# Kernel tuning notes

Hardware: AMD Instinct MI355X
Metric: run time of the kernel (lower is better)

Reference implementation:

```python
import jax, jax.numpy as jnp
import numpy as np

B, F, N, J, L_LAYERS = 16, 16, 1024, 8, 3


def setup_inputs() -> dict:
    key = jax.random.key(0)
    k1, k2, k3 = jax.random.split(key, 3)
    x = jax.random.normal(k1, (B, F, N), dtype=jnp.float32)
    psi = jax.random.normal(k2, (J, N, N), dtype=jnp.float32) / np.sqrt(N)
    lowpass = jax.random.uniform(k3, (N,), dtype=jnp.float32) / N
    return {"x": x, "psi": psi, "lowpass": lowpass, "L": L_LAYERS}


def reference(x, psi, lowpass, L):
    # x: [B, F, N] graph signals; psi: [J, N, N] wavelet filterbank; lowpass: [N]
    Bs, Fs, Ns = x.shape
    # layer-0 lowpass projection: phi = x @ lowpass -> [B, F, 1]
    phi = jnp.einsum('bfn,n->bf', x, lowpass)[:, :, None]
    S_x = x[:, None, :, :]  # [B, K=1, F, N]
    for _ in range(1, L):
        # apply all J wavelets to all K branches, then abs nonlinearity
        # (branch order k-major, j-minor matches the torch cat loop)
        S_x = jnp.abs(jnp.einsum('bkfn,jnm->bkjfm', S_x, psi))
        K = S_x.shape[1] * S_x.shape[2]
        S_x = S_x.reshape(Bs, K, Fs, Ns)
        # lowpass-pool every branch: [B, F, K]
        phi_l = jnp.einsum('bkfn,n->bfk', S_x, lowpass)
        phi = jnp.concatenate([phi, phi_l], axis=2)
    return phi  # [B, F, 1 + J + J^2 + ... + J^(L-1)]
```

## Files before the change

### kernel.cpp

```cpp
#include <hip/hip_runtime.h>

#define ND 1024
#define NNE (ND*ND)

typedef float f32x4 __attribute__((ext_vector_type(4)));
typedef int i32x4 __attribute__((ext_vector_type(4)));
typedef int i32x8 __attribute__((ext_vector_type(8)));

__device__ __forceinline__ void gload_lds16(const void* g, void* l) {
  __builtin_amdgcn_global_load_lds(
      (const __attribute__((address_space(1))) void*)g,
      (__attribute__((address_space(3))) void*)l, 16, 0, 0);
}

__global__ __launch_bounds__(256)
void prep_kernel(const float* __restrict__ psi, unsigned char* __restrict__ out8,
                 const float* __restrict__ x, const float* __restrict__ lp,
                 unsigned char* __restrict__ x8, float* __restrict__ phi) {
  __shared__ __align__(16) unsigned char T[128 * 144];
  __shared__ float ws[4];
  const int blk = blockIdx.x;
  const int tid = threadIdx.x;

  if (blk >= 512) {
    int row = blk - 512;
    if (tid >= 1 && tid < 73) phi[row * 73 + tid] = 0.f;
    float4 v = reinterpret_cast<const float4*>(x + (size_t)row * ND)[tid];
    float4 l = reinterpret_cast<const float4*>(lp)[tid];
    int pk = __builtin_amdgcn_cvt_pk_fp8_f32(v.x, v.y, 0, false);
    pk = __builtin_amdgcn_cvt_pk_fp8_f32(v.z, v.w, pk, true);
    reinterpret_cast<unsigned int*>(x8 + (size_t)row * ND)[tid] = (unsigned int)pk;
    float s = v.x * l.x + v.y * l.y + v.z * l.z + v.w * l.w;
    #pragma unroll
    for (int off = 32; off; off >>= 1) s += __shfl_xor(s, off);
    if ((tid & 63) == 0) ws[tid >> 6] = s;
    __syncthreads();
    if (tid == 0) phi[row * 73] = ws[0] + ws[1] + ws[2] + ws[3];
    return;
  }

  const int j  = blk >> 6;
  const int t6 = blk & 63;
  const int tn = t6 >> 3, tm = t6 & 7;
  const int n0 = tn * 128, m0 = tm * 128;
  const float* src = psi + ((size_t)j << 20) + (size_t)n0 * ND + m0;

  const int rgrp = tid >> 5;
  const int c4   = (tid & 31) << 2;
  #pragma unroll
  for (int it = 0; it < 16; ++it) {
    int nl = it * 8 + rgrp;
    float4 v = *reinterpret_cast<const float4*>(src + (size_t)nl * ND + c4);
    int p01 = __builtin_amdgcn_cvt_pk_fp8_f32(v.x, v.y, 0, false);
    int p23 = __builtin_amdgcn_cvt_pk_fp8_f32(v.z, v.w, 0, false);
    T[(c4 + 0) * 144 + nl] = (unsigned char)(p01 & 0xff);
    T[(c4 + 1) * 144 + nl] = (unsigned char)((p01 >> 8) & 0xff);
    T[(c4 + 2) * 144 + nl] = (unsigned char)(p23 & 0xff);
    T[(c4 + 3) * 144 + nl] = (unsigned char)((p23 >> 8) & 0xff);
  }
  __syncthreads();

  unsigned char* dst = out8 + ((size_t)j << 20) + (size_t)m0 * ND + n0;
  const int mrow = tid >> 3;
  const int ch   = (tid & 7) << 4;
  #pragma unroll
  for (int it = 0; it < 4; ++it) {
    int ml = it * 32 + mrow;
    uint4 v = *reinterpret_cast<const uint4*>(&T[ml * 144 + ch]);
    *reinterpret_cast<uint4*>(dst + (size_t)ml * ND + ch) = v;
  }
}

__device__ __forceinline__ i32x8 dsr_frag8(const unsigned char* base, int r, int l4) {
  int s0 = l4 * 2;
  i32x4 lo = *reinterpret_cast<const i32x4*>(base + r * 128 + ((s0 ^ (r & 7)) << 4));
  i32x4 hi = *reinterpret_cast<const i32x4*>(base + r * 128 + (((s0 + 1) ^ (r & 7)) << 4));
  return __builtin_shufflevector(lo, hi, 0, 1, 2, 3, 4, 5, 6, 7);
}

__global__ __launch_bounds__(256, 2)
void gemm8_l1(const unsigned char* __restrict__ A,
              const unsigned char* __restrict__ BT,
              const float* __restrict__ lowpass,
              unsigned char* __restrict__ Sout,
              float* __restrict__ phi) {
  __shared__ __align__(16) unsigned char As[128 * 128];
  __shared__ __align__(16) unsigned char Bs[128 * 128];

  const int tid  = threadIdx.x;
  const int lane = tid & 63;
  const int w    = tid >> 6;
  const int wrow = w >> 1, wcol = w & 1;
  const int l15  = lane & 15, l4 = lane >> 4;

  const int wg = blockIdx.x;
  const int j  = wg & 7;
  const int t  = wg >> 3;
  const int mtile = t & 1, ntile = t >> 1;
  const int row0 = mtile * 128, n0 = ntile * 128;
  const unsigned char* Bj = BT + (size_t)j * NNE;

  f32x4 acc[4][4] = {};

  #pragma unroll 1
  for (int k0 = 0; k0 < ND; k0 += 128) {
    __syncthreads();
    #pragma unroll
    for (int p = 0; p < 4; ++p) {
      int c = p * 256 + tid;
      int r = c >> 3;
      int s = (c & 7) ^ (r & 7);
      gload_lds16(A + (size_t)(row0 + r) * ND + k0 + (s << 4), As + c * 16);
    }
    #pragma unroll
    for (int p = 0; p < 4; ++p) {
      int c = p * 256 + tid;
      int r = c >> 3;
      int s = (c & 7) ^ (r & 7);
      gload_lds16(Bj + (size_t)(n0 + r) * ND + k0 + (s << 4), Bs + c * 16);
    }
    __syncthreads();

    i32x8 a[4], b[4];
    #pragma unroll
    for (int m = 0; m < 4; ++m)
      a[m] = dsr_frag8(As, wrow * 64 + m * 16 + l15, l4);
    #pragma unroll
    for (int n = 0; n < 4; ++n)
      b[n] = dsr_frag8(Bs, wcol * 64 + n * 16 + l15, l4);
    #pragma unroll
    for (int m = 0; m < 4; ++m)
      #pragma unroll
      for (int n = 0; n < 4; ++n)
        acc[m][n] = __builtin_amdgcn_mfma_scale_f32_16x16x128_f8f6f4(
            a[m], b[n], acc[m][n], 0, 0, 0, 0x7f7f7f7f, 0, 0x7f7f7f7f);
  }

  float lp[4];
  #pragma unroll
  for (int n = 0; n < 4; ++n)
    lp[n] = lowpass[n0 + wcol * 64 + n * 16 + l15];

  #pragma unroll
  for (int m = 0; m < 4; ++m) {
    #pragma unroll
    for (int r = 0; r < 4; ++r) {
      int rg = row0 + wrow * 64 + m * 16 + l4 * 4 + r;
      float psum = 0.f;
      #pragma unroll
      for (int n = 0; n < 4; ++n) {
        float v = fabsf(acc[m][n][r]);
        psum += v * lp[n];
        int colg = n0 + wcol * 64 + n * 16 + l15;
        size_t si = ((size_t)((rg >> 4) * 8 + j) * 16 + (rg & 15)) * ND + colg;
        int pk = __builtin_amdgcn_cvt_pk_fp8_f32(v, v, 0, false);
        Sout[si] = (unsigned char)(pk & 0xff);
      }
      psum += __shfl_xor(psum, 1);
      psum += __shfl_xor(psum, 2);
      psum += __shfl_xor(psum, 4);
      psum += __shfl_xor(psum, 8);
      if (l15 == 0) {
        int pidx = rg * 73 + 1 + j;
        atomicAdd(&phi[pidx], psum);
      }
    }
  }
}

__global__ __launch_bounds__(256, 2)
void gemm8_l2(const unsigned char* __restrict__ A,
              const unsigned char* __restrict__ BT,
              const float* __restrict__ lowpass,
              float* __restrict__ phi) {
  __shared__ __align__(16) unsigned char As[128 * 128];
  __shared__ __align__(16) unsigned char Bs[128 * 128];

  const int tid  = threadIdx.x;
  const int lane = tid & 63;
  const int w    = tid >> 6;
  const int wrow = w >> 1, wcol = w & 1;
  const int l15  = lane & 15, l4 = lane >> 4;

  const int wg  = blockIdx.x;
  const int j   = wg & 7;
  const int idx = wg >> 3;
  const unsigned char* Bj = BT + (size_t)j * NNE;

  #pragma unroll 1
  for (int tt = 0; tt < 2; ++tt) {
    const int t = idx + tt * 64;
    const int mtile = t & 15, ntile = t >> 4;
    const int row0 = mtile * 128, n0 = ntile * 128;

    f32x4 acc[4][4] = {};

    #pragma unroll 1
    for (int k0 = 0; k0 < ND; k0 += 128) {
      __syncthreads();
      #pragma unroll
      for (int p = 0; p < 4; ++p) {
        int c = p * 256 + tid;
        int r = c >> 3;
        int s = (c & 7) ^ (r & 7);
        gload_lds16(A + (size_t)(row0 + r) * ND + k0 + (s << 4), As + c * 16);
      }
      #pragma unroll
      for (int p = 0; p < 4; ++p) {
        int c = p * 256 + tid;
        int r = c >> 3;
        int s = (c & 7) ^ (r & 7);
        gload_lds16(Bj + (size_t)(n0 + r) * ND + k0 + (s << 4), Bs + c * 16);
      }
      __syncthreads();

      i32x8 a[4], b[4];
      #pragma unroll
      for (int m = 0; m < 4; ++m)
        a[m] = dsr_frag8(As, wrow * 64 + m * 16 + l15, l4);
      #pragma unroll
      for (int n = 0; n < 4; ++n)
        b[n] = dsr_frag8(Bs, wcol * 64 + n * 16 + l15, l4);
      #pragma unroll
      for (int m = 0; m < 4; ++m)
        #pragma unroll
        for (int n = 0; n < 4; ++n)
          acc[m][n] = __builtin_amdgcn_mfma_scale_f32_16x16x128_f8f6f4(
              a[m], b[n], acc[m][n], 0, 0, 0, 0x7f7f7f7f, 0, 0x7f7f7f7f);
    }

    float lp[4];
    #pragma unroll
    for (int n = 0; n < 4; ++n)
      lp[n] = lowpass[n0 + wcol * 64 + n * 16 + l15];

    #pragma unroll
    for (int m = 0; m < 4; ++m) {
      #pragma unroll
      for (int r = 0; r < 4; ++r) {
        int rg = row0 + wrow * 64 + m * 16 + l4 * 4 + r;
        float psum = 0.f;
        #pragma unroll
        for (int n = 0; n < 4; ++n)
          psum += fabsf(acc[m][n][r]) * lp[n];
        psum += __shfl_xor(psum, 1);
        psum += __shfl_xor(psum, 2);
        psum += __shfl_xor(psum, 4);
        psum += __shfl_xor(psum, 8);
        if (l15 == 0) {
          int pidx = ((rg >> 7) * 16 + (rg & 15)) * 73 + 9 + ((rg >> 4) & 7) * 8 + j;
          atomicAdd(&phi[pidx], psum);
        }
      }
    }
  }
}

extern "C" void kernel_launch(void* const* d_in, const int* in_sizes, int n_in,
                              void* d_out, int out_size, void* d_ws, size_t ws_size,
                              hipStream_t stream) {
  (void)in_sizes; (void)n_in; (void)ws_size; (void)out_size;
  const float* x       = (const float*)d_in[0];
  const float* psi     = (const float*)d_in[1];
  const float* lowpass = (const float*)d_in[2];
  float* phi = (float*)d_out;

  unsigned char* x8    = (unsigned char*)d_ws;
  unsigned char* psiT8 = (unsigned char*)((char*)d_ws + (1u << 20));
  unsigned char* S1f8  = (unsigned char*)((char*)d_ws + (10u << 20));

  prep_kernel<<<768, 256, 0, stream>>>(psi, psiT8, x, lowpass, x8, phi);

  gemm8_l1<<<128, 256, 0, stream>>>(x8, psiT8, lowpass, S1f8, phi);

  gemm8_l2<<<512, 256, 0, stream>>>(S1f8, psiT8, lowpass, phi);
}
```

Before: 64.37 us.

## Double-buffer LDS tiles in FP8 GEMM kernels to overlap loads with MFMA

Both gemm8 kernels now use two LDS buffers each for A and B. The next K-slice is issued via global_load_lds while the current slice is consumed by MFMA, and there is one barrier per iteration instead of two. The aim is to hide global-memory latency behind compute. LDS use doubles to 64KB per block, which may cut occupancy below the two blocks per CU requested in the launch bounds. The async loads also rely on the single barrier for completion, which is a potential race concern.

Measured after the change: 61.47 us. -4.5%, faster.

```diff
diff --git a/kernel.cpp b/kernel.cpp
--- a/kernel.cpp
+++ b/kernel.cpp
@@ -78,14 +78,54 @@
   return __builtin_shufflevector(lo, hi, 0, 1, 2, 3, 4, 5, 6, 7);
 }
 
+__device__ __forceinline__ void stage128(const unsigned char* __restrict__ A, int row0,
+                                         const unsigned char* __restrict__ Bj, int n0,
+                                         int k0, unsigned char* As, unsigned char* Bs,
+                                         int tid) {
+  #pragma unroll
+  for (int p = 0; p < 4; ++p) {
+    int c = p * 256 + tid;
+    int r = c >> 3;
+    int s = (c & 7) ^ (r & 7);
+    gload_lds16(A + (size_t)(row0 + r) * ND + k0 + (s << 4), As + c * 16);
+  }
+  #pragma unroll
+  for (int p = 0; p < 4; ++p) {
+    int c = p * 256 + tid;
+    int r = c >> 3;
+    int s = (c & 7) ^ (r & 7);
+    gload_lds16(Bj + (size_t)(n0 + r) * ND + k0 + (s << 4), Bs + c * 16);
+  }
+}
+
+__device__ __forceinline__ void compute128(const unsigned char* As, const unsigned char* Bs,
+                                           f32x4 (&acc)[4][4],
+                                           int wrow, int wcol, int l15, int l4) {
+  i32x8 a[4], b[4];
+  #pragma unroll
+  for (int m = 0; m < 4; ++m)
+    a[m] = dsr_frag8(As, wrow * 64 + m * 16 + l15, l4);
+  #pragma unroll
+  for (int n = 0; n < 4; ++n)
+    b[n] = dsr_frag8(Bs, wcol * 64 + n * 16 + l15, l4);
+  #pragma unroll
+  for (int m = 0; m < 4; ++m)
+    #pragma unroll
+    for (int n = 0; n < 4; ++n)
+      acc[m][n] = __builtin_amdgcn_mfma_scale_f32_16x16x128_f8f6f4(
+          a[m], b[n], acc[m][n], 0, 0, 0, 0x7f7f7f7f, 0, 0x7f7f7f7f);
+}
+
 __global__ __launch_bounds__(256, 2)
 void gemm8_l1(const unsigned char* __restrict__ A,
               const unsigned char* __restrict__ BT,
               const float* __restrict__ lowpass,
               unsigned char* __restrict__ Sout,
               float* __restrict__ phi) {
-  __shared__ __align__(16) unsigned char As[128 * 128];
-  __shared__ __align__(16) unsigned char Bs[128 * 128];
+  __shared__ __align__(16) unsigned char As0[128 * 128];
+  __shared__ __align__(16) unsigned char As1[128 * 128];
+  __shared__ __align__(16) unsigned char Bs0[128 * 128];
+  __shared__ __align__(16) unsigned char Bs1[128 * 128];
 
   const int tid  = threadIdx.x;
   const int lane = tid & 63;
@@ -102,38 +142,18 @@
 
   f32x4 acc[4][4] = {};
 
+  stage128(A, row0, Bj, n0, 0, As0, Bs0, tid);
+  __syncthreads();
+
   #pragma unroll 1
   for (int k0 = 0; k0 < ND; k0 += 128) {
+    const int cur = (k0 >> 7) & 1;
+    const unsigned char* Ac = cur ? As1 : As0;
+    const unsigned char* Bc = cur ? Bs1 : Bs0;
+    if (k0 + 128 < ND)
+      stage128(A, row0, Bj, n0, k0 + 128, cur ? As0 : As1, cur ? Bs0 : Bs1, tid);
+    compute128(Ac, Bc, acc, wrow, wcol, l15, l4);
     __syncthreads();
-    #pragma unroll
-    for (int p = 0; p < 4; ++p) {
-      int c = p * 256 + tid;
-      int r = c >> 3;
-      int s = (c & 7) ^ (r & 7);
-      gload_lds16(A + (size_t)(row0 + r) * ND + k0 + (s << 4), As + c * 16);
-    }
-    #pragma unroll
-    for (int p = 0; p < 4; ++p) {
-      int c = p * 256 + tid;
-      int r = c >> 3;
-      int s = (c & 7) ^ (r & 7);
-      gload_lds16(Bj + (size_t)(n0 + r) * ND + k0 + (s << 4), Bs + c * 16);
-    }
-    __syncthreads();
-
-    i32x8 a[4], b[4];
-    #pragma unroll
-    for (int m = 0; m < 4; ++m)
-      a[m] = dsr_frag8(As, wrow * 64 + m * 16 + l15, l4);
-    #pragma unroll
-    for (int n = 0; n < 4; ++n)
-      b[n] = dsr_frag8(Bs, wcol * 64 + n * 16 + l15, l4);
-    #pragma unroll
-    for (int m = 0; m < 4; ++m)
-      #pragma unroll
-      for (int n = 0; n < 4; ++n)
-        acc[m][n] = __builtin_amdgcn_mfma_scale_f32_16x16x128_f8f6f4(
-            a[m], b[n], acc[m][n], 0, 0, 0, 0x7f7f7f7f, 0, 0x7f7f7f7f);
   }
 
   float lp[4];
@@ -173,8 +193,10 @@
               const unsigned char* __restrict__ BT,
               const float* __restrict__ lowpass,
               float* __restrict__ phi) {
-  __shared__ __align__(16) unsigned char As[128 * 128];
-  __shared__ __align__(16) unsigned char Bs[128 * 128];
+  __shared__ __align__(16) unsigned char As0[128 * 128];
+  __shared__ __align__(16) unsigned char As1[128 * 128];
+  __shared__ __align__(16) unsigned char Bs0[128 * 128];
+  __shared__ __align__(16) unsigned char Bs1[128 * 128];
 
   const int tid  = threadIdx.x;
   const int lane = tid & 63;
@@ -195,38 +217,18 @@
 
     f32x4 acc[4][4] = {};
 
+    stage128(A, row0, Bj, n0, 0, As0, Bs0, tid);
+    __syncthreads();
+
     #pragma unroll 1
     for (int k0 = 0; k0 < ND; k0 += 128) {
+      const int cur = (k0 >> 7) & 1;
+      const unsigned char* Ac = cur ? As1 : As0;
+      const unsigned char* Bc = cur ? Bs1 : Bs0;
+      if (k0 + 128 < ND)
+        stage128(A, row0, Bj, n0, k0 + 128, cur ? As0 : As1, cur ? Bs0 : Bs1, tid);
+      compute128(Ac, Bc, acc, wrow, wcol, l15, l4);
       __syncthreads();
-      #pragma unroll
-      for (int p = 0; p < 4; ++p) {
-        int c = p * 256 + tid;
-        int r = c >> 3;
-        int s = (c & 7) ^ (r & 7);
-        gload_lds16(A + (size_t)(row0 + r) * ND + k0 + (s << 4), As + c * 16);
-      }
-      #pragma unroll
-      for (int p = 0; p < 4; ++p) {
-        int c = p * 256 + tid;
-        int r = c >> 3;
-        int s = (c & 7) ^ (r & 7);
-        gload_lds16(Bj + (size_t)(n0 + r) * ND + k0 + (s << 4), Bs + c * 16);
-      }
-      __syncthreads();
-
-      i32x8 a[4], b[4];
-      #pragma unroll
-      for (int m = 0; m < 4; ++m)
-        a[m] = dsr_frag8(As, wrow * 64 + m * 16 + l15, l4);
-      #pragma unroll
-      for (int n = 0; n < 4; ++n)
-        b[n] = dsr_frag8(Bs, wcol * 64 + n * 16 + l15, l4);
-      #pragma unroll
-      for (int m = 0; m < 4; ++m)
-        #pragma unroll
-        for (int n = 0; n < 4; ++n)
-          acc[m][n] = __builtin_amdgcn_mfma_scale_f32_16x16x128_f8f6f4(
-              a[m], b[n], acc[m][n], 0, 0, 0, 0x7f7f7f7f, 0, 0x7f7f7f7f);
     }
 
     float lp[4];
```
